# Performance work log

Hardware: AMD Instinct MI355X
Metric: run time of the kernel (lower is better)

The kernel has to match this reference:

```python
import jax, jax.numpy as jnp
import numpy as np

DIM, HEADS, K = 128, 4, 7
HD = DIM // HEADS


def _nbr_idx(n, k):
    # NATTEN boundary-clamped neighborhood (dilation=1): window start clamped to [0, n-k]
    i = np.arange(n)
    start = np.clip(i - k // 2, 0, n - k)
    idx = start[:, None] + np.arange(k)[None, :]          # (n, k) absolute neighbor index
    rel = idx - i[:, None] + (k - 1)                      # (n, k) index into 2k-1 rpb axis
    return jnp.asarray(idx), jnp.asarray(rel)


def _ln(x, w, b, eps=1e-5):
    mu = jnp.mean(x, -1, keepdims=True)
    var = jnp.var(x, -1, keepdims=True)
    return (x - mu) * jax.lax.rsqrt(var + eps) * w + b


def setup_inputs() -> dict:
    key = jax.random.key(0)
    ks = jax.random.split(key, 16)
    B, H, W, C = 1, 128, 128, DIM
    f = jax.random.normal
    inp = {
        'x': f(ks[0], (B, H, W, C), jnp.float32),
        'y': f(ks[1], (B, H, W, C), jnp.float32),
        'qv_w': f(ks[2], (2 * C, C), jnp.float32) * 0.02,
        'qv_b': jnp.zeros((2 * C,), jnp.float32),
        'k_w': f(ks[3], (C, C), jnp.float32) * 0.02,
        'k_b': jnp.zeros((C,), jnp.float32),
        'rpb': f(ks[4], (HEADS, 2 * K - 1, 2 * K - 1), jnp.float32) * 0.02,
        'proj_w': f(ks[5], (C, C), jnp.float32) * 0.02,
        'proj_b': jnp.zeros((C,), jnp.float32),
        'n1_w': jnp.ones((C,), jnp.float32),
        'n1_b': jnp.zeros((C,), jnp.float32),
        'n2_w': jnp.ones((C,), jnp.float32),
        'n2_b': jnp.zeros((C,), jnp.float32),
        'fc1_w': f(ks[6], (4 * C, C), jnp.float32) * 0.02,
        'fc1_b': jnp.zeros((4 * C,), jnp.float32),
        'fc2_w': f(ks[7], (C, 4 * C), jnp.float32) * 0.02,
        'fc2_b': jnp.zeros((C,), jnp.float32),
    }
    return inp


def _block(x, y, qv_w, qv_b, k_w, k_b, rpb, proj_w, proj_b,
           n1_w, n1_b, n2_w, n2_b, fc1_w, fc1_b, fc2_w, fc2_b):
    B, H, W, C = x.shape
    scale = HD ** -0.5
    # ---- CrossNat2D attention on norm1(x) vs y ----
    xn = _ln(x, n1_w, n1_b)
    qv = xn @ qv_w.T + qv_b                               # (B,H,W,2C)
    q = qv[..., :C].reshape(B, H, W, HEADS, HD) * scale
    v = qv[..., C:].reshape(B, H, W, HEADS, HD)
    k = (y @ k_w.T + k_b).reshape(B, H, W, HEADS, HD)

    idx_h, rel_h = _nbr_idx(H, K)
    idx_w, rel_w = _nbr_idx(W, K)
    # gather neighborhoods: (B, H, K, W, K, HEADS, HD)
    k_nbr = k[:, idx_h][:, :, :, idx_w]
    v_nbr = v[:, idx_h][:, :, :, idx_w]

    # attention logits over KxK neighborhood
    attn = jnp.einsum('bijhd,biajchd->bijhac', q, k_nbr)  # (B,H,W,heads,K,K)
    bias = rpb[:, rel_h][..., rel_w]                      # (heads,H,K,W,K)
    attn = attn + jnp.transpose(bias, (1, 3, 0, 2, 4))    # broadcast over B
    attn = jax.nn.softmax(attn.reshape(B, H, W, HEADS, K * K), axis=-1)
    attn = attn.reshape(B, H, W, HEADS, K, K)

    out = jnp.einsum('bijhac,biajchd->bijhd', attn, v_nbr).reshape(B, H, W, C)
    out = out @ proj_w.T + proj_b

    x = x + out
    # ---- MLP ----
    h = _ln(x, n2_w, n2_b) @ fc1_w.T + fc1_b
    h = jax.nn.gelu(h, approximate=False) @ fc2_w.T + fc2_b
    return x + h


def reference(x, y, qv_w, qv_b, k_w, k_b, rpb, proj_w, proj_b,
              n1_w, n1_b, n2_w, n2_b, fc1_w, fc1_b, fc2_w, fc2_b):
    return _block(x, y, qv_w, qv_b, k_w, k_b, rpb, proj_w, proj_b,
                  n1_w, n1_b, n2_w, n2_b, fc1_w, fc1_b, fc2_w, fc2_b)
```

## Files before the change

### kernel.cpp

```cpp
#include <hip/hip_runtime.h>
#include <hip/hip_bf16.h>


#define N_PIX 16384
#define C 128
#define HEADS 4
#define HD 32
#define HW 128

typedef __hip_bfloat16 bf16;
typedef __attribute__((ext_vector_type(8))) short bf16x8;
typedef __attribute__((ext_vector_type(4))) float f32x4;

__device__ __forceinline__ float b2f(bf16 v) { return __bfloat162float(v); }
__device__ __forceinline__ short f2bs(float f) {
    bf16 h = __float2bfloat16(f);
    return (short)__bfloat16_as_ushort(h);
}
__device__ __forceinline__ float bs2f(short s) {
    __hip_bfloat16_raw r; r.x = (unsigned short)s;
    return __bfloat162float(__hip_bfloat16(r));
}
__device__ __forceinline__ float gelu_f(float v) {
    const float z = 1.5957691216f * (v + 0.044715f * v * v * v);
    return v / (1.f + __expf(-z));
}

__global__ __launch_bounds__(256) void k_wconv(
    const float* __restrict__ qv_w, const float* __restrict__ k_w,
    const float* __restrict__ proj_w, const float* __restrict__ fc1_w,
    const float* __restrict__ fc2_w,
    short* __restrict__ wqv, short* __restrict__ wk, short* __restrict__ wproj,
    short* __restrict__ wfc1, short* __restrict__ wfc2) {
    const int i = blockIdx.x * 256 + threadIdx.x;
    if (i < 32768) wqv[i] = f2bs(qv_w[i]);
    if (i < 16384) { wk[i] = f2bs(k_w[i]); wproj[i] = f2bs(proj_w[i]); }
    if (i < 65536) { wfc1[i] = f2bs(fc1_w[i]); wfc2[i] = f2bs(fc2_w[i]); }
}

__global__ __launch_bounds__(512, 6) void k_qkv(
    const float* __restrict__ x, const float* __restrict__ y,
    const short* __restrict__ wqv, const float* __restrict__ qv_b,
    const short* __restrict__ wk, const float* __restrict__ k_b,
    const float* __restrict__ n1_w, const float* __restrict__ n1_b,
    bf16* __restrict__ qb, bf16* __restrict__ vb, bf16* __restrict__ kb) {
    __shared__ float xr[32][132];
    __shared__ short xn[32][136];
    __shared__ short yb[32][136];
    __shared__ float muA[32], riA[32];
    const int t = threadIdx.x;
    const int pix0 = blockIdx.x * 32;
    for (int e = t; e < 32 * 128; e += 512) {
        const int r = e >> 7, c = e & 127;
        xr[r][c] = x[(pix0 + r) * C + c];
        yb[r][c] = f2bs(y[(pix0 + r) * C + c]);
    }
    __syncthreads();
    if (t < 256) {
        const int r = t >> 3, s = t & 7;
        float sm = 0.f, sq = 0.f;
        for (int i = 0; i < 16; i++) { float v = xr[r][s * 16 + i]; sm += v; sq += v * v; }
        for (int m = 1; m < 8; m <<= 1) { sm += __shfl_xor(sm, m, 64); sq += __shfl_xor(sq, m, 64); }
        if (s == 0) {
            const float mu = sm * (1.f / 128.f);
            const float var = sq * (1.f / 128.f) - mu * mu;
            muA[r] = mu; riA[r] = rsqrtf(var + 1e-5f);
        }
    }
    __syncthreads();
    for (int e = t; e < 32 * 128; e += 512) {
        const int r = e >> 7, c = e & 127;
        xn[r][c] = f2bs((xr[r][c] - muA[r]) * riA[r] * n1_w[c] + n1_b[c]);
    }
    __syncthreads();
    const int wave = t >> 6, lane = t & 63, quad = lane >> 4, l15 = lane & 15;
    const float scale = 0.1767766952966369f;
    for (int jt = wave; jt < 48; jt += 8) {
        const int mt = jt & 1, nt = jt >> 1;
        f32x4 acc = {0.f, 0.f, 0.f, 0.f};
        if (nt < 16) {
            const int n = nt * 16 + l15;
            for (int kt = 0; kt < 4; kt++) {
                bf16x8 a = *(const bf16x8*)&xn[mt * 16 + l15][kt * 32 + quad * 8];
                bf16x8 b = *(const bf16x8*)&wqv[n * C + kt * 32 + quad * 8];
                acc = __builtin_amdgcn_mfma_f32_16x16x32_bf16(a, b, acc, 0, 0, 0);
            }
            const float bias = qv_b[n];
            for (int r = 0; r < 4; r++) {
                const int m = mt * 16 + quad * 4 + r;
                const float v = acc[r] + bias;
                if (n < C) qb[(pix0 + m) * C + n] = __float2bfloat16(v * scale);
                else       vb[(pix0 + m) * C + (n - C)] = __float2bfloat16(v);
            }
        } else {
            const int n = (nt - 16) * 16 + l15;
            for (int kt = 0; kt < 4; kt++) {
                bf16x8 a = *(const bf16x8*)&yb[mt * 16 + l15][kt * 32 + quad * 8];
                bf16x8 b = *(const bf16x8*)&wk[n * C + kt * 32 + quad * 8];
                acc = __builtin_amdgcn_mfma_f32_16x16x32_bf16(a, b, acc, 0, 0, 0);
            }
            const float bias = k_b[n];
            for (int r = 0; r < 4; r++) {
                const int m = mt * 16 + quad * 4 + r;
                kb[(pix0 + m) * C + n] = __float2bfloat16(acc[r] + bias);
            }
        }
    }
}

__global__ __launch_bounds__(256) void k_attn(
    const bf16* qb, const bf16* __restrict__ kb,
    const bf16* __restrict__ vb, const float* __restrict__ rpb,
    bf16* ao) {
    __shared__ short KP[100 * 132];
    __shared__ short Vl[100 * 132];
    const int t = threadIdx.x;
    const int h = t >> 6, lane = t & 63, quad = lane >> 4, l15 = lane & 15;
    const int i0 = (blockIdx.x >> 5) * 4;
    const int j0 = (blockIdx.x & 31) * 4;
    const int rs = min(max(i0 - 3, 0), 118);
    const int cs = min(max(j0 - 3, 0), 118);
    for (int u = t; u < 100 * 16 * 2; u += 256) {
        const int tv = (u >= 1600) ? 1 : 0;
        const int uu = tv ? u - 1600 : u;
        const int r = uu >> 4, seg = uu & 15;
        const int wr = r / 10, wc = r % 10;
        const size_t g = (size_t)((rs + wr) * HW + cs + wc) * C + seg * 8;
        const uint4 d = *(const uint4*)((tv ? vb : kb) + g);
        *(uint4*)&(tv ? Vl : KP)[r * 132 + seg * 8] = d;
    }
    __syncthreads();
    const int pA = (i0 + (l15 >> 2)) * HW + j0 + (l15 & 3);
    const bf16x8 aQ = *(const bf16x8*)(qb + (size_t)pA * C + h * HD + quad * 8);
    f32x4 S[7];
    int aiL[7], ajL[7]; bool inb[7];
    for (int nt = 0; nt < 7; nt++) {
        const int nb = nt * 16 + l15;
        aiL[nt] = rs + nb / 10;
        ajL[nt] = cs + nb % 10;
        inb[nt] = nb < 100;
        const bf16x8 bK = *(const bf16x8*)&KP[(nt * 16 + l15) * 132 + h * HD + quad * 8];
        f32x4 z = {0.f, 0.f, 0.f, 0.f};
        S[nt] = __builtin_amdgcn_mfma_f32_16x16x32_bf16(aQ, bK, z, 0, 0, 0);
    }
    const float* rpbh = rpb + h * 169;
    float sm[4];
    for (int r = 0; r < 4; r++) {
        const int m = quad * 4 + r;
        const int i = i0 + (m >> 2), j = j0 + (m & 3);
        const int shi = min(max(i - 3, 0), 121);
        const int swj = min(max(j - 3, 0), 121);
        float best = -1e30f;
        for (int nt = 0; nt < 7; nt++) {
            const int ai = aiL[nt], aj = ajL[nt];
            const bool valid = inb[nt] & (ai >= shi) & (ai <= shi + 6) & (aj >= swj) & (aj <= swj + 6);
            const int ri = min(max(ai - i + 6, 0), 12);
            const int rj = min(max(aj - j + 6, 0), 12);
            const float v = valid ? (S[nt][r] + rpbh[ri * 13 + rj]) : -1e30f;
            S[nt][r] = v;
            best = fmaxf(best, v);
        }
        for (int msk = 1; msk < 16; msk <<= 1) best = fmaxf(best, __shfl_xor(best, msk, 64));
        float s = 0.f;
        for (int nt = 0; nt < 7; nt++) {
            const float e = __expf(S[nt][r] - best);
            S[nt][r] = e;
            s += e;
        }
        for (int msk = 1; msk < 16; msk <<= 1) s += __shfl_xor(s, msk, 64);
        sm[r] = 1.f / s;
    }
    __syncthreads();
    for (int r = 0; r < 4; r++) {
        short* prow = &KP[(h * 16 + quad * 4 + r) * 136];
        for (int nt = 0; nt < 7; nt++)
            prow[nt * 16 + l15] = f2bs(S[nt][r] * sm[r]);
        prow[112 + l15] = 0;
    }
    __syncthreads();
    f32x4 O0 = {0.f, 0.f, 0.f, 0.f}, O1 = {0.f, 0.f, 0.f, 0.f};
    for (int kt = 0; kt < 4; kt++) {
        const bf16x8 aP = *(const bf16x8*)&KP[(h * 16 + l15) * 136 + kt * 32 + quad * 8];
        for (int nt2 = 0; nt2 < 2; nt2++) {
            bf16x8 bV;
            const int ch = h * HD + nt2 * 16 + l15;
#pragma unroll
            for (int jj = 0; jj < 8; jj++) {
                const int nbr = kt * 32 + quad * 8 + jj;
                bV[jj] = (nbr < 100) ? Vl[nbr * 132 + ch] : (short)0;
            }
            if (nt2 == 0) O0 = __builtin_amdgcn_mfma_f32_16x16x32_bf16(aP, bV, O0, 0, 0, 0);
            else          O1 = __builtin_amdgcn_mfma_f32_16x16x32_bf16(aP, bV, O1, 0, 0, 0);
        }
    }
    for (int r = 0; r < 4; r++) {
        const int m = quad * 4 + r;
        const int p = (i0 + (m >> 2)) * HW + j0 + (m & 3);
        ao[(size_t)p * C + h * HD + l15] = __float2bfloat16(O0[r]);
        ao[(size_t)p * C + h * HD + 16 + l15] = __float2bfloat16(O1[r]);
    }
}

__global__ __launch_bounds__(512, 6) void k_mlp2(
    const float* __restrict__ x, const bf16* __restrict__ ao,
    const short* __restrict__ wproj, const float* __restrict__ proj_b,
    const float* __restrict__ n2_w, const float* __restrict__ n2_b,
    const short* __restrict__ wfc1, const float* __restrict__ fc1_b,
    const short* __restrict__ wfc2, const float* __restrict__ fc2_b,
    float* __restrict__ out) {
    __shared__ short x1b[32][136];
    __shared__ short xn[32][136];
    __shared__ short hb[32][520];
    __shared__ float muA[32], riA[32];
    const int t = threadIdx.x;
    const int pix0 = blockIdx.x * 32;
    const int wave = t >> 6, lane = t & 63, quad = lane >> 4, l15 = lane & 15;
    for (int jt = wave; jt < 16; jt += 8) {
        const int mt = jt >> 3, nt = jt & 7;
        const int n = nt * 16 + l15;
        const bf16* aop = ao + (size_t)(pix0 + mt * 16 + l15) * C;
        f32x4 acc = {0.f, 0.f, 0.f, 0.f};
        for (int kt = 0; kt < 4; kt++) {
            bf16x8 a = *(const bf16x8*)(aop + kt * 32 + quad * 8);
            bf16x8 b = *(const bf16x8*)&wproj[n * C + kt * 32 + quad * 8];
            acc = __builtin_amdgcn_mfma_f32_16x16x32_bf16(a, b, acc, 0, 0, 0);
        }
        const float bias = proj_b[n];
        for (int r = 0; r < 4; r++) {
            const int m = mt * 16 + quad * 4 + r;
            x1b[m][n] = f2bs(x[(pix0 + m) * C + n] + acc[r] + bias);
        }
    }
    __syncthreads();
    if (t < 256) {
        const int r = t >> 3, s = t & 7;
        float sm = 0.f, sq = 0.f;
        for (int i = 0; i < 16; i++) { float v = bs2f(x1b[r][s * 16 + i]); sm += v; sq += v * v; }
        for (int m = 1; m < 8; m <<= 1) { sm += __shfl_xor(sm, m, 64); sq += __shfl_xor(sq, m, 64); }
        if (s == 0) {
            const float mu = sm * (1.f / 128.f);
            const float var = sq * (1.f / 128.f) - mu * mu;
            muA[r] = mu; riA[r] = rsqrtf(var + 1e-5f);
        }
    }
    __syncthreads();
    for (int e = t; e < 32 * 128; e += 512) {
        const int r = e >> 7, c = e & 127;
        xn[r][c] = f2bs((bs2f(x1b[r][c]) - muA[r]) * riA[r] * n2_w[c] + n2_b[c]);
    }
    __syncthreads();
    for (int jt = wave; jt < 64; jt += 8) {
        const int mt = jt >> 5, nt = jt & 31;
        const int n = nt * 16 + l15;
        f32x4 acc = {0.f, 0.f, 0.f, 0.f};
        for (int kt = 0; kt < 4; kt++) {
            bf16x8 a = *(const bf16x8*)&xn[mt * 16 + l15][kt * 32 + quad * 8];
            bf16x8 b = *(const bf16x8*)&wfc1[n * C + kt * 32 + quad * 8];
            acc = __builtin_amdgcn_mfma_f32_16x16x32_bf16(a, b, acc, 0, 0, 0);
        }
        const float bias = fc1_b[n];
        for (int r = 0; r < 4; r++) {
            const int m = mt * 16 + quad * 4 + r;
            hb[m][n] = f2bs(gelu_f(acc[r] + bias));
        }
    }
    __syncthreads();
    for (int jt = wave; jt < 16; jt += 8) {
        const int mt = jt >> 3, nt = jt & 7;
        const int n = nt * 16 + l15;
        f32x4 acc = {0.f, 0.f, 0.f, 0.f};
#pragma unroll
        for (int kt = 0; kt < 16; kt++) {
            bf16x8 a = *(const bf16x8*)&hb[mt * 16 + l15][kt * 32 + quad * 8];
            bf16x8 b = *(const bf16x8*)&wfc2[n * 512 + kt * 32 + quad * 8];
            acc = __builtin_amdgcn_mfma_f32_16x16x32_bf16(a, b, acc, 0, 0, 0);
        }
        const float bias = fc2_b[n];
        for (int r = 0; r < 4; r++) {
            const int m = mt * 16 + quad * 4 + r;
            out[(pix0 + m) * C + n] = acc[r] + bias + bs2f(x1b[m][n]);
        }
    }
}

extern "C" void kernel_launch(void* const* d_in, const int* in_sizes, int n_in,
                              void* d_out, int out_size, void* d_ws, size_t ws_size,
                              hipStream_t stream) {
    const float* x      = (const float*)d_in[0];
    const float* y      = (const float*)d_in[1];
    const float* qv_w   = (const float*)d_in[2];
    const float* qv_b   = (const float*)d_in[3];
    const float* k_w    = (const float*)d_in[4];
    const float* k_b    = (const float*)d_in[5];
    const float* rpb    = (const float*)d_in[6];
    const float* proj_w = (const float*)d_in[7];
    const float* proj_b = (const float*)d_in[8];
    const float* n1_w   = (const float*)d_in[9];
    const float* n1_b   = (const float*)d_in[10];
    const float* n2_w   = (const float*)d_in[11];
    const float* n2_b   = (const float*)d_in[12];
    const float* fc1_w  = (const float*)d_in[13];
    const float* fc1_b  = (const float*)d_in[14];
    const float* fc2_w  = (const float*)d_in[15];
    const float* fc2_b  = (const float*)d_in[16];
    float* out = (float*)d_out;

    bf16* qb  = (bf16*)d_ws;
    bf16* vb  = qb + (size_t)N_PIX * C;
    bf16* kb  = vb + (size_t)N_PIX * C;
    short* wqv  = (short*)(kb + (size_t)N_PIX * C);
    short* wk   = wqv + 32768;
    short* wproj= wk + 16384;
    short* wfc1 = wproj + 16384;
    short* wfc2 = wfc1 + 65536;
    bf16* ao = qb;

    k_wconv<<<256, 256, 0, stream>>>(qv_w, k_w, proj_w, fc1_w, fc2_w,
                                     wqv, wk, wproj, wfc1, wfc2);
    k_qkv<<<N_PIX / 32, 512, 0, stream>>>(x, y, wqv, qv_b, wk, k_b, n1_w, n1_b, qb, vb, kb);
    k_attn<<<1024, 256, 0, stream>>>(qb, kb, vb, rpb, ao);
    k_mlp2<<<N_PIX / 32, 512, 0, stream>>>(x, ao, wproj, proj_b, n2_w, n2_b,
                                           wfc1, fc1_b, wfc2, fc2_b, out);
}
```

Baseline: 173.7 us.

## Fuse neighborhood attention with projection and MLP into one kernel

Merges the attention kernel and the proj+LN+MLP kernel so each 4x4 pixel tile computes its attention output into shared memory and immediately applies projection, residual, LayerNorm, fc1/GELU and fc2. This removes the global write and re-read of the attention output and one kernel launch. In exchange, each block now processes only 16 pixels with 4 waves, so the weight matrices are re-read from cache twice as often per pixel and MLP parallelism per block drops. Shared memory buffers are aliased to reuse the K/V staging space.

New measurement: 173.1 us. Within noise of the previous version (-0.3%).

```diff
diff --git a/kernel.cpp b/kernel.cpp
--- a/kernel.cpp
+++ b/kernel.cpp
@@ -12,7 +12,6 @@
 typedef __attribute__((ext_vector_type(8))) short bf16x8;
 typedef __attribute__((ext_vector_type(4))) float f32x4;
 
-__device__ __forceinline__ float b2f(bf16 v) { return __bfloat162float(v); }
 __device__ __forceinline__ short f2bs(float f) {
     bf16 h = __float2bfloat16(f);
     return (short)__bfloat16_as_ushort(h);
@@ -108,12 +107,23 @@
     }
 }
 
-__global__ __launch_bounds__(256) void k_attn(
-    const bf16* qb, const bf16* __restrict__ kb,
+__global__ __launch_bounds__(256) void k_fam(
+    const bf16* __restrict__ qb, const bf16* __restrict__ kb,
     const bf16* __restrict__ vb, const float* __restrict__ rpb,
-    bf16* ao) {
-    __shared__ short KP[100 * 132];
-    __shared__ short Vl[100 * 132];
+    const float* __restrict__ x,
+    const short* __restrict__ wproj, const float* __restrict__ proj_b,
+    const float* __restrict__ n2_w, const float* __restrict__ n2_b,
+    const short* __restrict__ wfc1, const float* __restrict__ fc1_b,
+    const short* __restrict__ wfc2, const float* __restrict__ fc2_b,
+    float* __restrict__ out) {
+    __shared__ short KP[13200];
+    __shared__ short Vl[13200];
+    __shared__ float muA[16], riA[16];
+    short* const Pm  = KP;
+    short* const aoL = KP + 8704;
+    short* const x1b = KP + 10880;
+    short* const hb  = Vl;
+    short* const xnb = Vl + 8320;
     const int t = threadIdx.x;
     const int h = t >> 6, lane = t & 63, quad = lane >> 4, l15 = lane & 15;
     const int i0 = (blockIdx.x >> 5) * 4;
@@ -124,8 +134,7 @@
         const int tv = (u >= 1600) ? 1 : 0;
         const int uu = tv ? u - 1600 : u;
         const int r = uu >> 4, seg = uu & 15;
-        const int wr = r / 10, wc = r % 10;
-        const size_t g = (size_t)((rs + wr) * HW + cs + wc) * C + seg * 8;
+        const size_t g = (size_t)((rs + r / 10) * HW + cs + r % 10) * C + seg * 8;
         const uint4 d = *(const uint4*)((tv ? vb : kb) + g);
         *(uint4*)&(tv ? Vl : KP)[r * 132 + seg * 8] = d;
     }
@@ -144,7 +153,7 @@
         S[nt] = __builtin_amdgcn_mfma_f32_16x16x32_bf16(aQ, bK, z, 0, 0, 0);
     }
     const float* rpbh = rpb + h * 169;
-    float sm[4];
+    float smx[4];
     for (int r = 0; r < 4; r++) {
         const int m = quad * 4 + r;
         const int i = i0 + (m >> 2), j = j0 + (m & 3);
@@ -168,19 +177,19 @@
             s += e;
         }
         for (int msk = 1; msk < 16; msk <<= 1) s += __shfl_xor(s, msk, 64);
-        sm[r] = 1.f / s;
+        smx[r] = 1.f / s;
     }
     __syncthreads();
     for (int r = 0; r < 4; r++) {
-        short* prow = &KP[(h * 16 + quad * 4 + r) * 136];
+        short* prow = &Pm[(h * 16 + quad * 4 + r) * 136];
         for (int nt = 0; nt < 7; nt++)
-            prow[nt * 16 + l15] = f2bs(S[nt][r] * sm[r]);
+            prow[nt * 16 + l15] = f2bs(S[nt][r] * smx[r]);
         prow[112 + l15] = 0;
     }
     __syncthreads();
     f32x4 O0 = {0.f, 0.f, 0.f, 0.f}, O1 = {0.f, 0.f, 0.f, 0.f};
     for (int kt = 0; kt < 4; kt++) {
-        const bf16x8 aP = *(const bf16x8*)&KP[(h * 16 + l15) * 136 + kt * 32 + quad * 8];
+        const bf16x8 aP = *(const bf16x8*)&Pm[(h * 16 + l15) * 136 + kt * 32 + quad * 8];
         for (int nt2 = 0; nt2 < 2; nt2++) {
             bf16x8 bV;
             const int ch = h * HD + nt2 * 16 + l15;
@@ -195,47 +204,30 @@
     }
     for (int r = 0; r < 4; r++) {
         const int m = quad * 4 + r;
-        const int p = (i0 + (m >> 2)) * HW + j0 + (m & 3);
-        ao[(size_t)p * C + h * HD + l15] = __float2bfloat16(O0[r]);
-        ao[(size_t)p * C + h * HD + 16 + l15] = __float2bfloat16(O1[r]);
-    }
-}
-
-__global__ __launch_bounds__(512, 6) void k_mlp2(
-    const float* __restrict__ x, const bf16* __restrict__ ao,
-    const short* __restrict__ wproj, const float* __restrict__ proj_b,
-    const float* __restrict__ n2_w, const float* __restrict__ n2_b,
-    const short* __restrict__ wfc1, const float* __restrict__ fc1_b,
-    const short* __restrict__ wfc2, const float* __restrict__ fc2_b,
-    float* __restrict__ out) {
-    __shared__ short x1b[32][136];
-    __shared__ short xn[32][136];
-    __shared__ short hb[32][520];
-    __shared__ float muA[32], riA[32];
-    const int t = threadIdx.x;
-    const int pix0 = blockIdx.x * 32;
-    const int wave = t >> 6, lane = t & 63, quad = lane >> 4, l15 = lane & 15;
-    for (int jt = wave; jt < 16; jt += 8) {
-        const int mt = jt >> 3, nt = jt & 7;
-        const int n = nt * 16 + l15;
-        const bf16* aop = ao + (size_t)(pix0 + mt * 16 + l15) * C;
+        aoL[m * 136 + h * HD + l15] = f2bs(O0[r]);
+        aoL[m * 136 + h * HD + 16 + l15] = f2bs(O1[r]);
+    }
+    __syncthreads();
+    for (int jt = h; jt < 8; jt += 4) {
+        const int n = jt * 16 + l15;
         f32x4 acc = {0.f, 0.f, 0.f, 0.f};
         for (int kt = 0; kt < 4; kt++) {
-            bf16x8 a = *(const bf16x8*)(aop + kt * 32 + quad * 8);
+            bf16x8 a = *(const bf16x8*)&aoL[l15 * 136 + kt * 32 + quad * 8];
             bf16x8 b = *(const bf16x8*)&wproj[n * C + kt * 32 + quad * 8];
             acc = __builtin_amdgcn_mfma_f32_16x16x32_bf16(a, b, acc, 0, 0, 0);
         }
         const float bias = proj_b[n];
         for (int r = 0; r < 4; r++) {
-            const int m = mt * 16 + quad * 4 + r;
-            x1b[m][n] = f2bs(x[(pix0 + m) * C + n] + acc[r] + bias);
-        }
-    }
-    __syncthreads();
-    if (t < 256) {
+            const int m = quad * 4 + r;
+            const int p = (i0 + (m >> 2)) * HW + j0 + (m & 3);
+            x1b[m * 136 + n] = f2bs(x[(size_t)p * C + n] + acc[r] + bias);
+        }
+    }
+    __syncthreads();
+    if (t < 128) {
         const int r = t >> 3, s = t & 7;
         float sm = 0.f, sq = 0.f;
-        for (int i = 0; i < 16; i++) { float v = bs2f(x1b[r][s * 16 + i]); sm += v; sq += v * v; }
+        for (int i = 0; i < 16; i++) { float v = bs2f(x1b[r * 136 + s * 16 + i]); sm += v; sq += v * v; }
         for (int m = 1; m < 8; m <<= 1) { sm += __shfl_xor(sm, m, 64); sq += __shfl_xor(sq, m, 64); }
         if (s == 0) {
             const float mu = sm * (1.f / 128.f);
@@ -244,41 +236,38 @@
         }
     }
     __syncthreads();
-    for (int e = t; e < 32 * 128; e += 512) {
+    for (int e = t; e < 16 * 128; e += 256) {
         const int r = e >> 7, c = e & 127;
-        xn[r][c] = f2bs((bs2f(x1b[r][c]) - muA[r]) * riA[r] * n2_w[c] + n2_b[c]);
-    }
-    __syncthreads();
-    for (int jt = wave; jt < 64; jt += 8) {
-        const int mt = jt >> 5, nt = jt & 31;
-        const int n = nt * 16 + l15;
+        xnb[r * 136 + c] = f2bs((bs2f(x1b[r * 136 + c]) - muA[r]) * riA[r] * n2_w[c] + n2_b[c]);
+    }
+    __syncthreads();
+    for (int jt = h; jt < 32; jt += 4) {
+        const int n = jt * 16 + l15;
         f32x4 acc = {0.f, 0.f, 0.f, 0.f};
         for (int kt = 0; kt < 4; kt++) {
-            bf16x8 a = *(const bf16x8*)&xn[mt * 16 + l15][kt * 32 + quad * 8];
+            bf16x8 a = *(const bf16x8*)&xnb[l15 * 136 + kt * 32 + quad * 8];
             bf16x8 b = *(const bf16x8*)&wfc1[n * C + kt * 32 + quad * 8];
             acc = __builtin_amdgcn_mfma_f32_16x16x32_bf16(a, b, acc, 0, 0, 0);
         }
         const float bias = fc1_b[n];
-        for (int r = 0; r < 4; r++) {
-            const int m = mt * 16 + quad * 4 + r;
-            hb[m][n] = f2bs(gelu_f(acc[r] + bias));
-        }
-    }
-    __syncthreads();
-    for (int jt = wave; jt < 16; jt += 8) {
-        const int mt = jt >> 3, nt = jt & 7;
-        const int n = nt * 16 + l15;
+        for (int r = 0; r < 4; r++)
+            hb[(quad * 4 + r) * 520 + n] = f2bs(gelu_f(acc[r] + bias));
+    }
+    __syncthreads();
+    for (int jt = h; jt < 8; jt += 4) {
+        const int n = jt * 16 + l15;
         f32x4 acc = {0.f, 0.f, 0.f, 0.f};
 #pragma unroll
         for (int kt = 0; kt < 16; kt++) {
-            bf16x8 a = *(const bf16x8*)&hb[mt * 16 + l15][kt * 32 + quad * 8];
+            bf16x8 a = *(const bf16x8*)&hb[l15 * 520 + kt * 32 + quad * 8];
             bf16x8 b = *(const bf16x8*)&wfc2[n * 512 + kt * 32 + quad * 8];
             acc = __builtin_amdgcn_mfma_f32_16x16x32_bf16(a, b, acc, 0, 0, 0);
         }
         const float bias = fc2_b[n];
         for (int r = 0; r < 4; r++) {
-            const int m = mt * 16 + quad * 4 + r;
-            out[(pix0 + m) * C + n] = acc[r] + bias + bs2f(x1b[m][n]);
+            const int m = quad * 4 + r;
+            const int p = (i0 + (m >> 2)) * HW + j0 + (m & 3);
+            out[(size_t)p * C + n] = acc[r] + bias + bs2f(x1b[m * 136 + n]);
         }
     }
 }
@@ -313,12 +302,10 @@
     short* wproj= wk + 16384;
     short* wfc1 = wproj + 16384;
     short* wfc2 = wfc1 + 65536;
-    bf16* ao = qb;
 
     k_wconv<<<256, 256, 0, stream>>>(qv_w, k_w, proj_w, fc1_w, fc2_w,
                                      wqv, wk, wproj, wfc1, wfc2);
     k_qkv<<<N_PIX / 32, 512, 0, stream>>>(x, y, wqv, qv_b, wk, k_b, n1_w, n1_b, qb, vb, kb);
-    k_attn<<<1024, 256, 0, stream>>>(qb, kb, vb, rpb, ao);
-    k_mlp2<<<N_PIX / 32, 512, 0, stream>>>(x, ao, wproj, proj_b, n2_w, n2_b,
-                                           wfc1, fc1_b, wfc2, fc2_b, out);
-}
+    k_fam<<<1024, 256, 0, stream>>>(qb, kb, vb, rpb, x, wproj, proj_b, n2_w, n2_b,
+                                    wfc1, fc1_b, wfc2, fc2_b, out);
+}
```
